# Performance work log

Hardware: AMD Instinct MI355X
Metric: run time of the kernel (lower is better)

The kernel has to match this reference:

```python
import jax, jax.numpy as jnp
import numpy as np

D_MODEL = 1024
SEQ_LEN = 4096


def setup_inputs() -> dict:
    key = jax.random.key(0)
    ks = jax.random.split(key, 7)
    s = 1.0 / np.sqrt(D_MODEL)
    return {
        "x": jax.random.normal(ks[0], (SEQ_LEN, D_MODEL), dtype=jnp.float32),
        "w_q": jax.random.normal(ks[1], (D_MODEL, D_MODEL), dtype=jnp.float32) * s,
        "b_q": jax.random.normal(ks[2], (D_MODEL,), dtype=jnp.float32) * s,
        "w_k": jax.random.normal(ks[3], (D_MODEL, D_MODEL), dtype=jnp.float32) * s,
        "b_k": jax.random.normal(ks[4], (D_MODEL,), dtype=jnp.float32) * s,
        "w_v": jax.random.normal(ks[5], (D_MODEL, D_MODEL), dtype=jnp.float32) * s,
        "b_v": jax.random.normal(ks[6], (D_MODEL,), dtype=jnp.float32) * s,
    }


def reference(x, w_q, b_q, w_k, b_k, w_v, b_v):
    # q/k/v: [S, D]; torch Linear computes x @ W.T + b, weights here stored as [D, D]
    q = x @ w_q.T + b_q
    k = x @ w_k.T + b_k
    v = x @ w_v.T + b_v
    temperature = jnp.asarray(D_MODEL, dtype=x.dtype) ** 0.5
    # scores: [S, S]
    attn = jax.nn.softmax((q / temperature) @ k.T, axis=-1)
    # dropout is identity in eval mode
    return attn @ v
```

## Files before the change

kernel.cpp:

```cpp
#include <hip/hip_runtime.h>
#include <hip/hip_bf16.h>
#include <stdint.h>

#define SEQ 4096
#define DM  1024

typedef __attribute__((ext_vector_type(8))) short  s16x8;
typedef __attribute__((ext_vector_type(8))) _Float16 h16x8;
typedef __attribute__((ext_vector_type(4))) float  f32x4;

__device__ __forceinline__ ushort f2bf(float f) {
    union { float f; uint32_t u; } x; x.f = f;
    uint32_t r = x.u + 0x7fffu + ((x.u >> 16) & 1u);
    return (ushort)(r >> 16);
}

__device__ __forceinline__ void gload16(const void* g, void* l) {
    __builtin_amdgcn_global_load_lds(
        (const __attribute__((address_space(1))) void*)g,
        (__attribute__((address_space(3))) void*)l,
        16, 0, 0);
}

__global__ __launch_bounds__(256)
void cvt_all(const float* __restrict__ x,  const float* __restrict__ wq,
             const float* __restrict__ wk, const float* __restrict__ wv,
             ushort* __restrict__ xb,  ushort* __restrict__ wqb,
             ushort* __restrict__ wkb, ushort* __restrict__ wvb)
{
    int i = blockIdx.x * 256 + threadIdx.x;
    const float* src; ushort* dst; int k;
    if (i < 1048576) { src = x; dst = xb; k = i; }
    else {
        int j = i - 1048576; int w = j >> 18; k = j & 262143;
        src = (w == 0) ? wq : (w == 1) ? wk : wv;
        dst = (w == 0) ? wqb : (w == 1) ? wkb : wvb;
    }
    float4 v = ((const float4*)src)[k];
    ushort4 o;
    o.x = f2bf(v.x); o.y = f2bf(v.y); o.z = f2bf(v.z); o.w = f2bf(v.w);
    ((ushort4*)dst)[k] = o;
}

template<int MODE>
__global__ __launch_bounds__(512, 1)
void gemm256p(const ushort* __restrict__ pA,  const ushort* __restrict__ pB,  void* __restrict__ pC,
              const ushort* __restrict__ pA2, const ushort* __restrict__ pB2, void* __restrict__ pC2,
              const ushort* __restrict__ pA3, const ushort* __restrict__ pB3, void* __restrict__ pC3,
              const float* __restrict__ pb1,  const float* __restrict__ pb2,  const float* __restrict__ pb3)
{
    constexpr int BN      = (MODE == 1) ? 128 : 256;
    constexpr int WN      = BN / 4;
    constexpr int NJ      = BN / 64;
    constexpr int LDA     = (MODE == 1) ? 4096 : 1024;
    constexpr int REG_A   = 16384;
    constexpr int REG_B   = BN * 64;
    constexpr int BUFSZ   = 2 * (REG_A + REG_B);
    constexpr int NTILES  = (MODE == 1) ? 32 : 16;
    constexpr int TOTAL_H = NTILES * 4;
    constexpr int NWG     = (MODE == 2) ? 192 : 256;

    __shared__ alignas(16) char lb[2 * BUFSZ];

    const int wg = blockIdx.x;
    const int logical = (wg & 7) * (NWG / 8) + (wg >> 3);

    int m0, n0, ldc_ = 0, biasRow = 0;
    const ushort *Ab, *Bb;
    char* Cc;
    const float* bias = nullptr;
    float scale = 1.0f;

    if constexpr (MODE == 0) {
        const int bx = logical & 15, by = logical >> 4;
        m0 = by * 256; n0 = bx * 256;
        Ab = pA + (size_t)m0 * LDA; Bb = pB + (size_t)n0 * LDA;
        Cc = (char*)pC; ldc_ = 4096;
    } else if constexpr (MODE == 1) {
        const int t = logical >> 1, ks = logical & 1;
        m0 = (t >> 3) * 256; n0 = (t & 7) * 128;
        Ab = pA + (size_t)m0 * LDA + ks * 2048;
        Bb = pB + (size_t)n0 * LDA + ks * 2048;
        Cc = (char*)pC + (size_t)ks * 8388608u;
        ldc_ = 1024;
    } else {
        const int which = logical / 64, t = logical % 64;
        if (which == 0)      { m0 = (t >> 2) * 256; n0 = (t & 3) * 256;  Ab = pA;  Bb = pB;  Cc = (char*)pC;  bias = pb1; scale = 0.03125f; ldc_ = 1024; }
        else if (which == 1) { m0 = (t >> 2) * 256; n0 = (t & 3) * 256;  Ab = pA2; Bb = pB2; Cc = (char*)pC2; bias = pb2; ldc_ = 1024; }
        else                 { m0 = (t >> 4) * 256; n0 = (t & 15) * 256; Ab = pA3; Bb = pB3; Cc = (char*)pC3; bias = pb3; biasRow = 1; ldc_ = 4096; }
        Ab += (size_t)m0 * LDA; Bb += (size_t)n0 * LDA;
    }

    const int tid = threadIdx.x;
    const int w = tid >> 6, l = tid & 63;
    const int wr = w >> 2, wc = w & 3;
    const int lm = l & 15;
    const int khb = (l >> 4) * 16;

    const int in0 = tid * 16, in1 = 8192 + tid * 16;
    const int b0 = in0 ^ (((in0 >> 9) & 1) << 5);
    const int b1 = in1 ^ (((in1 >> 9) & 1) << 5);
    const int r0_ = b0 >> 6, c0_ = (b0 & 63) >> 1;
    const int r1_ = b1 >> 6, c1_ = (b1 & 63) >> 1;

    const int swzb = ((lm >> 3) & 1) << 5;
    const int aoff = (((wr * 128 + lm) * 64 + khb) ^ swzb);
    const int boff = (((wc * WN  + lm) * 64 + khb) ^ swzb);

    f32x4 acc[8][NJ] = {};
    s16x8 bqr[NJ];

    constexpr int AR0 = 0, BR0 = REG_A, AR1 = REG_A + REG_B, BR1 = 2 * REG_A + REG_B;

#define ROFFX(reg_) ((reg_) == 0 ? AR0 : (reg_) == 1 ? BR0 : (reg_) == 2 ? AR1 : BR1)

#define STAGE_H(g) do { \
    const int hidx_ = (g) - 1, tile_ = hidx_ >> 2, reg_ = hidx_ & 3; \
    const int colb_ = tile_ * 64 + (reg_ >> 1) * 32; \
    char* dst_ = lb + (tile_ & 1) * BUFSZ + ROFFX(reg_); \
    if (reg_ & 1) { \
        gload16(Bb + (size_t)r0_ * LDA + colb_ + c0_, dst_ + in0); \
        if (BN == 256) gload16(Bb + (size_t)r1_ * LDA + colb_ + c1_, dst_ + in1); \
    } else { \
        gload16(Ab + (size_t)r0_ * LDA + colb_ + c0_, dst_ + in0); \
        gload16(Ab + (size_t)r1_ * LDA + colb_ + c1_, dst_ + in1); \
    } \
} while (0)

#define PHASE8(ph, kt2, VC) do { \
    constexpr int kk_ = (((ph) - 1) >> 1) & 1; \
    constexpr int mh_ = ((ph) - 1) & 1; \
    constexpr int rbuf_ = ((ph) <= 4) ? 0 : 1; \
    constexpr int aro_ = kk_ ? AR1 : AR0; \
    constexpr int bro_ = kk_ ? BR1 : BR0; \
    s16x8 aq[4]; \
    if (mh_ == 0) { \
        _Pragma("unroll") \
        for (int nj = 0; nj < NJ; ++nj) \
            bqr[nj] = *(const s16x8*)(lb + rbuf_ * BUFSZ + bro_ + boff + nj * 1024); \
    } \
    _Pragma("unroll") \
    for (int i = 0; i < 4; ++i) \
        aq[i] = *(const s16x8*)(lb + rbuf_ * BUFSZ + aro_ + aoff + (mh_ * 4 + i) * 1024); \
    { const int g_ = (kt2) * 8 + (ph) + 6; if (g_ <= TOTAL_H) STAGE_H(g_); } \
    asm volatile("s_waitcnt lgkmcnt(0)" ::: "memory"); \
    __builtin_amdgcn_sched_barrier(0); \
    __builtin_amdgcn_s_setprio(1); \
    _Pragma("unroll") \
    for (int i = 0; i < 4; ++i) { \
        _Pragma("unroll") \
        for (int nj = 0; nj < NJ; ++nj) \
            acc[mh_ * 4 + i][nj] = __builtin_amdgcn_mfma_f32_16x16x32_bf16( \
                aq[i], bqr[nj], acc[mh_ * 4 + i][nj], 0, 0, 0); \
    } \
    __builtin_amdgcn_s_setprio(0); \
    if ((ph) == 4 || (ph) == 8) asm volatile("s_waitcnt vmcnt(" #VC ")" ::: "memory"); \
    __builtin_amdgcn_s_barrier(); \
} while (0)

#define MPHASE(q, kt2, VC) do { \
    constexpr int kk_ = ((q) - 1) & 1; \
    constexpr int rbuf_ = ((q) <= 2) ? 0 : 1; \
    constexpr int aro_ = kk_ ? AR1 : AR0; \
    constexpr int bro_ = kk_ ? BR1 : BR0; \
    s16x8 aq[8]; \
    _Pragma("unroll") \
    for (int nj = 0; nj < NJ; ++nj) \
        bqr[nj] = *(const s16x8*)(lb + rbuf_ * BUFSZ + bro_ + boff + nj * 1024); \
    _Pragma("unroll") \
    for (int i = 0; i < 8; ++i) \
        aq[i] = *(const s16x8*)(lb + rbuf_ * BUFSZ + aro_ + aoff + i * 1024); \
    { const int g1_ = (kt2) * 8 + 2 * (q) + 5; if (g1_ <= TOTAL_H) STAGE_H(g1_); \
      const int g2_ = g1_ + 1;                 if (g2_ <= TOTAL_H) STAGE_H(g2_); } \
    asm volatile("s_waitcnt lgkmcnt(0)" ::: "memory"); \
    __builtin_amdgcn_sched_barrier(0); \
    __builtin_amdgcn_s_setprio(1); \
    _Pragma("unroll") \
    for (int i = 0; i < 8; ++i) { \
        _Pragma("unroll") \
        for (int nj = 0; nj < NJ; ++nj) \
            acc[i][nj] = __builtin_amdgcn_mfma_f32_16x16x32_bf16( \
                aq[i], bqr[nj], acc[i][nj], 0, 0, 0); \
    } \
    __builtin_amdgcn_s_setprio(0); \
    if ((q) == 2 || (q) == 4) asm volatile("s_waitcnt vmcnt(" #VC ")" ::: "memory"); \
    __builtin_amdgcn_s_barrier(); \
} while (0)

    STAGE_H(1); STAGE_H(2); STAGE_H(3); STAGE_H(4); STAGE_H(5); STAGE_H(6);
    if constexpr (MODE == 1) asm volatile("s_waitcnt vmcnt(3)" ::: "memory");
    else                     asm volatile("s_waitcnt vmcnt(4)" ::: "memory");
    __builtin_amdgcn_s_barrier();

    if constexpr (MODE == 1) {
        for (int kt2 = 0; kt2 < NTILES / 2 - 1; ++kt2) {
            MPHASE(1, kt2, 3); MPHASE(2, kt2, 3); MPHASE(3, kt2, 3); MPHASE(4, kt2, 3);
        }
        { const int kt2 = NTILES / 2 - 1;
          MPHASE(1, kt2, 0); MPHASE(2, kt2, 0); MPHASE(3, kt2, 0); MPHASE(4, kt2, 0); }
    } else {
        for (int kt2 = 0; kt2 < NTILES / 2 - 1; ++kt2) {
            PHASE8(1, kt2, 4); PHASE8(2, kt2, 4); PHASE8(3, kt2, 4); PHASE8(4, kt2, 4);
            PHASE8(5, kt2, 4); PHASE8(6, kt2, 4); PHASE8(7, kt2, 4); PHASE8(8, kt2, 4);
        }
        { const int kt2 = NTILES / 2 - 1;
          PHASE8(1, kt2, 0); PHASE8(2, kt2, 0); PHASE8(3, kt2, 0); PHASE8(4, kt2, 0);
          PHASE8(5, kt2, 0); PHASE8(6, kt2, 0); PHASE8(7, kt2, 0); PHASE8(8, kt2, 0); }
    }

    const int er0 = m0 + wr * 128 + (l >> 4) * 4;
    const int ec0 = n0 + wc * WN + lm;
#pragma unroll
    for (int mi = 0; mi < 8; ++mi) {
#pragma unroll
        for (int nj = 0; nj < NJ; ++nj) {
#pragma unroll
            for (int r = 0; r < 4; ++r) {
                const int row = er0 + mi * 16 + r;
                const int col = ec0 + nj * 16;
                if constexpr (MODE == 2) {
                    const float v = (acc[mi][nj][r] + bias[biasRow ? row : col]) * scale;
                    ((ushort*)Cc)[(size_t)row * ldc_ + col] = f2bf(v);
                } else {
                    ((_Float16*)Cc)[(size_t)row * ldc_ + col] = (_Float16)acc[mi][nj][r];
                }
            }
        }
    }
#undef MPHASE
#undef PHASE8
#undef STAGE_H
#undef ROFFX
}

__global__ __launch_bounds__(256) void softmax_rows(void* __restrict__ Sbase) {
    const int row = blockIdx.x;
    const int tid = threadIdx.x;
    const _Float16* srow = (const _Float16*)Sbase + (size_t)row * SEQ;

    float f[16];
#pragma unroll
    for (int j = 0; j < 2; ++j) {
        h16x8 v = *(const h16x8*)(srow + (size_t)(tid + j * 256) * 8);
#pragma unroll
        for (int e = 0; e < 8; ++e) f[j * 8 + e] = (float)v[e];
    }

    float m = f[0];
#pragma unroll
    for (int i = 1; i < 16; ++i) m = fmaxf(m, f[i]);
#pragma unroll
    for (int off = 32; off > 0; off >>= 1) m = fmaxf(m, __shfl_xor(m, off));

    __shared__ float redm[4], reds[4];
    const int w = tid >> 6, l = tid & 63;
    if (l == 0) redm[w] = m;
    __syncthreads();
    m = fmaxf(fmaxf(redm[0], redm[1]), fmaxf(redm[2], redm[3]));

    float s = 0.f;
#pragma unroll
    for (int i = 0; i < 16; ++i) { f[i] = __expf(f[i] - m); s += f[i]; }
#pragma unroll
    for (int off = 32; off > 0; off >>= 1) s += __shfl_xor(s, off);
    if (l == 0) reds[w] = s;
    __syncthreads();
    s = (reds[0] + reds[1]) + (reds[2] + reds[3]);
    const float inv = 1.0f / s;

    ushort* prow = (ushort*)Sbase + (size_t)row * SEQ;
#pragma unroll
    for (int j = 0; j < 2; ++j) {
        s16x8 o;
#pragma unroll
        for (int e = 0; e < 8; ++e) o[e] = (short)f2bf(f[j * 8 + e] * inv);
        *(s16x8*)(prow + (size_t)(tid + j * 256) * 8) = o;
    }
}

__global__ __launch_bounds__(256)
void reduce2(const _Float16* __restrict__ p0, const _Float16* __restrict__ p1,
             float* __restrict__ out)
{
    const size_t i = (size_t)(blockIdx.x * 256 + threadIdx.x) * 8;
    h16x8 a = *(const h16x8*)(p0 + i);
    h16x8 b = *(const h16x8*)(p1 + i);
    float4 o0, o1;
    o0.x = (float)a[0] + (float)b[0]; o0.y = (float)a[1] + (float)b[1];
    o0.z = (float)a[2] + (float)b[2]; o0.w = (float)a[3] + (float)b[3];
    o1.x = (float)a[4] + (float)b[4]; o1.y = (float)a[5] + (float)b[5];
    o1.z = (float)a[6] + (float)b[6]; o1.w = (float)a[7] + (float)b[7];
    *(float4*)(out + i) = o0;
    *(float4*)(out + i + 4) = o1;
}

extern "C" void kernel_launch(void* const* d_in, const int* in_sizes, int n_in,
                              void* d_out, int out_size, void* d_ws, size_t ws_size,
                              hipStream_t stream)
{
    const float* x  = (const float*)d_in[0];
    const float* wq = (const float*)d_in[1];
    const float* bq = (const float*)d_in[2];
    const float* wk = (const float*)d_in[3];
    const float* bk = (const float*)d_in[4];
    const float* wv = (const float*)d_in[5];
    const float* bv = (const float*)d_in[6];

    char* ws = (char*)d_ws;
    const size_t MB = 1024 * 1024;
    ushort*   Qb  = (ushort*)(ws);
    ushort*   Kb  = (ushort*)(ws + 8 * MB);
    ushort*   Vt  = (ushort*)(ws + 16 * MB);
    void*     Sm  = (void*)(ws + 24 * MB);
    ushort*   P   = (ushort*)(ws + 24 * MB);
    ushort*   xb  = (ushort*)(ws + 24 * MB);
    ushort*   wqb = (ushort*)(ws + 32 * MB);
    ushort*   wkb = (ushort*)(ws + 34 * MB);
    ushort*   wvb = (ushort*)(ws + 36 * MB);
    _Float16* Pp  = (_Float16*)(ws);

    cvt_all<<<dim3(7168), dim3(256), 0, stream>>>(x, wq, wk, wv, xb, wqb, wkb, wvb);

    gemm256p<2><<<dim3(192), dim3(512), 0, stream>>>(
        xb, wqb, Qb, xb, wkb, Kb, wvb, xb, Vt, bq, bk, bv);

    gemm256p<0><<<dim3(256), dim3(512), 0, stream>>>(
        Qb, Kb, Sm, nullptr, nullptr, nullptr, nullptr, nullptr, nullptr,
        nullptr, nullptr, nullptr);

    softmax_rows<<<dim3(SEQ), dim3(256), 0, stream>>>(Sm);

    gemm256p<1><<<dim3(256), dim3(512), 0, stream>>>(
        P, Vt, Pp, nullptr, nullptr, nullptr, nullptr, nullptr, nullptr,
        nullptr, nullptr, nullptr);

    reduce2<<<dim3(2048), dim3(256), 0, stream>>>(Pp, Pp + (size_t)4096 * 1024,
                                                  (float*)d_out);
}
```

Before: 133.1 us.

## Use 128x128-tile GEMM kernel for QK^T and PV, grid-stride softmax

Adds a new gemm128p kernel (256 threads, 128x128 tiles, two blocks per CU) and uses it for the QK^T score GEMM and the split-K PV GEMM, replacing the 256-tile MODE 0/1 paths. The original 256-tile kernel is now kept only for the fused QKV projection. Softmax now runs on 2048 blocks that each loop over two rows. Smaller tiles give more workgroups and better occupancy on the many CUs, at the cost of less operand reuse per tile and more global and LDS traffic.

```diff
diff --git a/kernel.cpp b/kernel.cpp
--- a/kernel.cpp
+++ b/kernel.cpp
@@ -49,16 +49,16 @@
               const ushort* __restrict__ pA3, const ushort* __restrict__ pB3, void* __restrict__ pC3,
               const float* __restrict__ pb1,  const float* __restrict__ pb2,  const float* __restrict__ pb3)
 {
-    constexpr int BN      = (MODE == 1) ? 128 : 256;
+    constexpr int BN      = 256;
     constexpr int WN      = BN / 4;
     constexpr int NJ      = BN / 64;
-    constexpr int LDA     = (MODE == 1) ? 4096 : 1024;
+    constexpr int LDA     = 1024;
     constexpr int REG_A   = 16384;
     constexpr int REG_B   = BN * 64;
     constexpr int BUFSZ   = 2 * (REG_A + REG_B);
-    constexpr int NTILES  = (MODE == 1) ? 32 : 16;
+    constexpr int NTILES  = 16;
     constexpr int TOTAL_H = NTILES * 4;
-    constexpr int NWG     = (MODE == 2) ? 192 : 256;
+    constexpr int NWG     = 192;
 
     __shared__ alignas(16) char lb[2 * BUFSZ];
 
@@ -71,19 +71,7 @@
     const float* bias = nullptr;
     float scale = 1.0f;
 
-    if constexpr (MODE == 0) {
-        const int bx = logical & 15, by = logical >> 4;
-        m0 = by * 256; n0 = bx * 256;
-        Ab = pA + (size_t)m0 * LDA; Bb = pB + (size_t)n0 * LDA;
-        Cc = (char*)pC; ldc_ = 4096;
-    } else if constexpr (MODE == 1) {
-        const int t = logical >> 1, ks = logical & 1;
-        m0 = (t >> 3) * 256; n0 = (t & 7) * 128;
-        Ab = pA + (size_t)m0 * LDA + ks * 2048;
-        Bb = pB + (size_t)n0 * LDA + ks * 2048;
-        Cc = (char*)pC + (size_t)ks * 8388608u;
-        ldc_ = 1024;
-    } else {
+    {
         const int which = logical / 64, t = logical % 64;
         if (which == 0)      { m0 = (t >> 2) * 256; n0 = (t & 3) * 256;  Ab = pA;  Bb = pB;  Cc = (char*)pC;  bias = pb1; scale = 0.03125f; ldc_ = 1024; }
         else if (which == 1) { m0 = (t >> 2) * 256; n0 = (t & 3) * 256;  Ab = pA2; Bb = pB2; Cc = (char*)pC2; bias = pb2; ldc_ = 1024; }
@@ -120,7 +108,7 @@
     char* dst_ = lb + (tile_ & 1) * BUFSZ + ROFFX(reg_); \
     if (reg_ & 1) { \
         gload16(Bb + (size_t)r0_ * LDA + colb_ + c0_, dst_ + in0); \
-        if (BN == 256) gload16(Bb + (size_t)r1_ * LDA + colb_ + c1_, dst_ + in1); \
+        gload16(Bb + (size_t)r1_ * LDA + colb_ + c1_, dst_ + in1); \
     } else { \
         gload16(Ab + (size_t)r0_ * LDA + colb_ + c0_, dst_ + in0); \
         gload16(Ab + (size_t)r1_ * LDA + colb_ + c1_, dst_ + in1); \
@@ -158,27 +146,123 @@
     __builtin_amdgcn_s_barrier(); \
 } while (0)
 
-#define MPHASE(q, kt2, VC) do { \
+    STAGE_H(1); STAGE_H(2); STAGE_H(3); STAGE_H(4); STAGE_H(5); STAGE_H(6);
+    asm volatile("s_waitcnt vmcnt(4)" ::: "memory");
+    __builtin_amdgcn_s_barrier();
+
+    for (int kt2 = 0; kt2 < NTILES / 2 - 1; ++kt2) {
+        PHASE8(1, kt2, 4); PHASE8(2, kt2, 4); PHASE8(3, kt2, 4); PHASE8(4, kt2, 4);
+        PHASE8(5, kt2, 4); PHASE8(6, kt2, 4); PHASE8(7, kt2, 4); PHASE8(8, kt2, 4);
+    }
+    { const int kt2 = NTILES / 2 - 1;
+      PHASE8(1, kt2, 0); PHASE8(2, kt2, 0); PHASE8(3, kt2, 0); PHASE8(4, kt2, 0);
+      PHASE8(5, kt2, 0); PHASE8(6, kt2, 0); PHASE8(7, kt2, 0); PHASE8(8, kt2, 0); }
+
+    const int er0 = m0 + wr * 128 + (l >> 4) * 4;
+    const int ec0 = n0 + wc * WN + lm;
+#pragma unroll
+    for (int mi = 0; mi < 8; ++mi) {
+#pragma unroll
+        for (int nj = 0; nj < NJ; ++nj) {
+#pragma unroll
+            for (int r = 0; r < 4; ++r) {
+                const int row = er0 + mi * 16 + r;
+                const int col = ec0 + nj * 16;
+                const float v = (acc[mi][nj][r] + bias[biasRow ? row : col]) * scale;
+                ((ushort*)Cc)[(size_t)row * ldc_ + col] = f2bf(v);
+            }
+        }
+    }
+#undef PHASE8
+#undef STAGE_H
+#undef ROFFX
+}
+
+template<int IS_PV>
+__global__ __launch_bounds__(256, 2)
+void gemm128p(const ushort* __restrict__ A, const ushort* __restrict__ B,
+              _Float16* __restrict__ C)
+{
+    constexpr int LDA     = IS_PV ? 4096 : 1024;
+    constexpr int LDC     = IS_PV ? 1024 : 4096;
+    constexpr int NTILES  = IS_PV ? 32 : 16;
+    constexpr int TOTAL_H = NTILES * 4;
+    constexpr int REG     = 8192;
+    constexpr int BUFSZ   = 4 * REG;
+    __shared__ alignas(16) char lb[2 * BUFSZ];
+
+    const int wg = blockIdx.x;
+    int m0, n0;
+    const ushort *Ab, *Bb;
+    _Float16* Cc;
+    if constexpr (!IS_PV) {
+        const int logical = (wg & 7) * 128 + (wg >> 3);
+        const int bx = logical & 31, by = logical >> 5;
+        m0 = by * 128; n0 = bx * 128;
+        Ab = A + (size_t)m0 * LDA; Bb = B + (size_t)n0 * LDA; Cc = C;
+    } else {
+        const int logical = (wg & 7) * 64 + (wg >> 3);
+        const int ks = logical & 1, t = logical >> 1;
+        const int by = t >> 3, bx = t & 7;
+        m0 = by * 128; n0 = bx * 128;
+        Ab = A + (size_t)m0 * LDA + ks * 2048;
+        Bb = B + (size_t)n0 * LDA + ks * 2048;
+        Cc = C + (size_t)ks * 4194304u;
+    }
+
+    const int tid = threadIdx.x;
+    const int w = tid >> 6, l = tid & 63;
+    const int wm = (w >> 1) * 64, wn = (w & 1) * 64;
+    const int lm = l & 15;
+    const int khb = (l >> 4) * 16;
+
+    const int in0 = tid * 16, in1 = 4096 + tid * 16;
+    const int b0 = in0 ^ (((in0 >> 9) & 1) << 5);
+    const int b1 = in1 ^ (((in1 >> 9) & 1) << 5);
+    const int r0_ = b0 >> 6, c0_ = (b0 & 63) >> 1;
+    const int r1_ = b1 >> 6, c1_ = (b1 & 63) >> 1;
+
+    const int swzb = ((lm >> 3) & 1) << 5;
+    const int aoff = ((wm + lm) * 64 + khb) ^ swzb;
+    const int boff = ((wn + lm) * 64 + khb) ^ swzb;
+
+    f32x4 acc[4][4] = {};
+    s16x8 bqr[4];
+
+    constexpr int AR0 = 0, BR0 = REG, AR1 = 2 * REG, BR1 = 3 * REG;
+
+#define ROFF3(reg_) ((reg_) == 0 ? AR0 : (reg_) == 1 ? BR0 : (reg_) == 2 ? AR1 : BR1)
+
+#define STAGE3(g) do { \
+    const int hidx_ = (g) - 1, tile_ = hidx_ >> 2, reg_ = hidx_ & 3; \
+    const int colb_ = tile_ * 64 + (reg_ >> 1) * 32; \
+    char* dst_ = lb + (tile_ & 1) * BUFSZ + ROFF3(reg_); \
+    const ushort* mp_ = (reg_ & 1) ? Bb : Ab; \
+    gload16(mp_ + (size_t)r0_ * LDA + colb_ + c0_, dst_ + in0); \
+    gload16(mp_ + (size_t)r1_ * LDA + colb_ + c1_, dst_ + in1); \
+} while (0)
+
+#define MP3(q, kt2, VC) do { \
     constexpr int kk_ = ((q) - 1) & 1; \
     constexpr int rbuf_ = ((q) <= 2) ? 0 : 1; \
     constexpr int aro_ = kk_ ? AR1 : AR0; \
     constexpr int bro_ = kk_ ? BR1 : BR0; \
-    s16x8 aq[8]; \
+    s16x8 aq[4]; \
     _Pragma("unroll") \
-    for (int nj = 0; nj < NJ; ++nj) \
+    for (int nj = 0; nj < 4; ++nj) \
         bqr[nj] = *(const s16x8*)(lb + rbuf_ * BUFSZ + bro_ + boff + nj * 1024); \
     _Pragma("unroll") \
-    for (int i = 0; i < 8; ++i) \
+    for (int i = 0; i < 4; ++i) \
         aq[i] = *(const s16x8*)(lb + rbuf_ * BUFSZ + aro_ + aoff + i * 1024); \
-    { const int g1_ = (kt2) * 8 + 2 * (q) + 5; if (g1_ <= TOTAL_H) STAGE_H(g1_); \
-      const int g2_ = g1_ + 1;                 if (g2_ <= TOTAL_H) STAGE_H(g2_); } \
+    { const int g1_ = (kt2) * 8 + 2 * (q) + 5; if (g1_ <= TOTAL_H) STAGE3(g1_); \
+      const int g2_ = g1_ + 1;                 if (g2_ <= TOTAL_H) STAGE3(g2_); } \
     asm volatile("s_waitcnt lgkmcnt(0)" ::: "memory"); \
     __builtin_amdgcn_sched_barrier(0); \
     __builtin_amdgcn_s_setprio(1); \
     _Pragma("unroll") \
-    for (int i = 0; i < 8; ++i) { \
+    for (int i = 0; i < 4; ++i) { \
         _Pragma("unroll") \
-        for (int nj = 0; nj < NJ; ++nj) \
+        for (int nj = 0; nj < 4; ++nj) \
             acc[i][nj] = __builtin_amdgcn_mfma_f32_16x16x32_bf16( \
                 aq[i], bqr[nj], acc[i][nj], 0, 0, 0); \
     } \
@@ -187,94 +271,76 @@
     __builtin_amdgcn_s_barrier(); \
 } while (0)
 
-    STAGE_H(1); STAGE_H(2); STAGE_H(3); STAGE_H(4); STAGE_H(5); STAGE_H(6);
-    if constexpr (MODE == 1) asm volatile("s_waitcnt vmcnt(3)" ::: "memory");
-    else                     asm volatile("s_waitcnt vmcnt(4)" ::: "memory");
+    STAGE3(1); STAGE3(2); STAGE3(3); STAGE3(4); STAGE3(5); STAGE3(6);
+    asm volatile("s_waitcnt vmcnt(4)" ::: "memory");
     __builtin_amdgcn_s_barrier();
 
-    if constexpr (MODE == 1) {
-        for (int kt2 = 0; kt2 < NTILES / 2 - 1; ++kt2) {
-            MPHASE(1, kt2, 3); MPHASE(2, kt2, 3); MPHASE(3, kt2, 3); MPHASE(4, kt2, 3);
+    for (int kt2 = 0; kt2 < NTILES / 2 - 1; ++kt2) {
+        MP3(1, kt2, 4); MP3(2, kt2, 4); MP3(3, kt2, 4); MP3(4, kt2, 4);
+    }
+    { const int kt2 = NTILES / 2 - 1;
+      MP3(1, kt2, 0); MP3(2, kt2, 0); MP3(3, kt2, 0); MP3(4, kt2, 0); }
+
+    const int er0 = m0 + wm + ((l >> 4) << 2);
+    const int ec0 = n0 + wn + lm;
+#pragma unroll
+    for (int mi = 0; mi < 4; ++mi)
+#pragma unroll
+        for (int nj = 0; nj < 4; ++nj)
+#pragma unroll
+            for (int r = 0; r < 4; ++r)
+                Cc[(size_t)(er0 + mi * 16 + r) * LDC + ec0 + nj * 16] =
+                    (_Float16)acc[mi][nj][r];
+#undef MP3
+#undef STAGE3
+#undef ROFF3
+}
+
+__global__ __launch_bounds__(256) void softmax_rows(void* __restrict__ Sbase) {
+    const int tid = threadIdx.x;
+    const int w = tid >> 6, l = tid & 63;
+    __shared__ float redm[4], reds[4];
+
+    for (int row = blockIdx.x; row < SEQ; row += 2048) {
+        const _Float16* srow = (const _Float16*)Sbase + (size_t)row * SEQ;
+
+        float f[16];
+#pragma unroll
+        for (int j = 0; j < 2; ++j) {
+            h16x8 v = *(const h16x8*)(srow + (size_t)(tid + j * 256) * 8);
+#pragma unroll
+            for (int e = 0; e < 8; ++e) f[j * 8 + e] = (float)v[e];
         }
-        { const int kt2 = NTILES / 2 - 1;
-          MPHASE(1, kt2, 0); MPHASE(2, kt2, 0); MPHASE(3, kt2, 0); MPHASE(4, kt2, 0); }
-    } else {
-        for (int kt2 = 0; kt2 < NTILES / 2 - 1; ++kt2) {
-            PHASE8(1, kt2, 4); PHASE8(2, kt2, 4); PHASE8(3, kt2, 4); PHASE8(4, kt2, 4);
-            PHASE8(5, kt2, 4); PHASE8(6, kt2, 4); PHASE8(7, kt2, 4); PHASE8(8, kt2, 4);
+
+        float m = f[0];
+#pragma unroll
+        for (int i = 1; i < 16; ++i) m = fmaxf(m, f[i]);
+#pragma unroll
+        for (int off = 32; off > 0; off >>= 1) m = fmaxf(m, __shfl_xor(m, off));
+
+        if (l == 0) redm[w] = m;
+        __syncthreads();
+        m = fmaxf(fmaxf(redm[0], redm[1]), fmaxf(redm[2], redm[3]));
+
+        float s = 0.f;
+#pragma unroll
+        for (int i = 0; i < 16; ++i) { f[i] = __expf(f[i] - m); s += f[i]; }
+#pragma unroll
+        for (int off = 32; off > 0; off >>= 1) s += __shfl_xor(s, off);
+        if (l == 0) reds[w] = s;
+        __syncthreads();
+        s = (reds[0] + reds[1]) + (reds[2] + reds[3]);
+        const float inv = 1.0f / s;
+
+        ushort* prow = (ushort*)Sbase + (size_t)row * SEQ;
+#pragma unroll
+        for (int j = 0; j < 2; ++j) {
+            s16x8 o;
+#pragma unroll
+            for (int e = 0; e < 8; ++e) o[e] = (short)f2bf(f[j * 8 + e] * inv);
+            *(s16x8*)(prow + (size_t)(tid + j * 256) * 8) = o;
         }
-        { const int kt2 = NTILES / 2 - 1;
-          PHASE8(1, kt2, 0); PHASE8(2, kt2, 0); PHASE8(3, kt2, 0); PHASE8(4, kt2, 0);
-          PHASE8(5, kt2, 0); PHASE8(6, kt2, 0); PHASE8(7, kt2, 0); PHASE8(8, kt2, 0); }
-    }
-
-    const int er0 = m0 + wr * 128 + (l >> 4) * 4;
-    const int ec0 = n0 + wc * WN + lm;
-#pragma unroll
-    for (int mi = 0; mi < 8; ++mi) {
-#pragma unroll
-        for (int nj = 0; nj < NJ; ++nj) {
-#pragma unroll
-            for (int r = 0; r < 4; ++r) {
-                const int row = er0 + mi * 16 + r;
-                const int col = ec0 + nj * 16;
-                if constexpr (MODE == 2) {
-                    const float v = (acc[mi][nj][r] + bias[biasRow ? row : col]) * scale;
-                    ((ushort*)Cc)[(size_t)row * ldc_ + col] = f2bf(v);
-                } else {
-                    ((_Float16*)Cc)[(size_t)row * ldc_ + col] = (_Float16)acc[mi][nj][r];
-                }
-            }
-        }
-    }
-#undef MPHASE
-#undef PHASE8
-#undef STAGE_H
-#undef ROFFX
-}
-
-__global__ __launch_bounds__(256) void softmax_rows(void* __restrict__ Sbase) {
-    const int row = blockIdx.x;
-    const int tid = threadIdx.x;
-    const _Float16* srow = (const _Float16*)Sbase + (size_t)row * SEQ;
-
-    float f[16];
-#pragma unroll
-    for (int j = 0; j < 2; ++j) {
-        h16x8 v = *(const h16x8*)(srow + (size_t)(tid + j * 256) * 8);
-#pragma unroll
-        for (int e = 0; e < 8; ++e) f[j * 8 + e] = (float)v[e];
-    }
-
-    float m = f[0];
-#pragma unroll
-    for (int i = 1; i < 16; ++i) m = fmaxf(m, f[i]);
-#pragma unroll
-    for (int off = 32; off > 0; off >>= 1) m = fmaxf(m, __shfl_xor(m, off));
-
-    __shared__ float redm[4], reds[4];
-    const int w = tid >> 6, l = tid & 63;
-    if (l == 0) redm[w] = m;
-    __syncthreads();
-    m = fmaxf(fmaxf(redm[0], redm[1]), fmaxf(redm[2], redm[3]));
-
-    float s = 0.f;
-#pragma unroll
-    for (int i = 0; i < 16; ++i) { f[i] = __expf(f[i] - m); s += f[i]; }
-#pragma unroll
-    for (int off = 32; off > 0; off >>= 1) s += __shfl_xor(s, off);
-    if (l == 0) reds[w] = s;
-    __syncthreads();
-    s = (reds[0] + reds[1]) + (reds[2] + reds[3]);
-    const float inv = 1.0f / s;
-
-    ushort* prow = (ushort*)Sbase + (size_t)row * SEQ;
-#pragma unroll
-    for (int j = 0; j < 2; ++j) {
-        s16x8 o;
-#pragma unroll
-        for (int e = 0; e < 8; ++e) o[e] = (short)f2bf(f[j * 8 + e] * inv);
-        *(s16x8*)(prow + (size_t)(tid + j * 256) * 8) = o;
+        __syncthreads();
     }
 }
 
@@ -324,15 +390,11 @@
     gemm256p<2><<<dim3(192), dim3(512), 0, stream>>>(
         xb, wqb, Qb, xb, wkb, Kb, wvb, xb, Vt, bq, bk, bv);
 
-    gemm256p<0><<<dim3(256), dim3(512), 0, stream>>>(
-        Qb, Kb, Sm, nullptr, nullptr, nullptr, nullptr, nullptr, nullptr,
-        nullptr, nullptr, nullptr);
-
-    softmax_rows<<<dim3(SEQ), dim3(256), 0, stream>>>(Sm);
-
-    gemm256p<1><<<dim3(256), dim3(512), 0, stream>>>(
-        P, Vt, Pp, nullptr, nullptr, nullptr, nullptr, nullptr, nullptr,
-        nullptr, nullptr, nullptr);
+    gemm128p<0><<<dim3(1024), dim3(256), 0, stream>>>(Qb, Kb, (_Float16*)Sm);
+
+    softmax_rows<<<dim3(2048), dim3(256), 0, stream>>>(Sm);
+
+    gemm128p<1><<<dim3(512), dim3(256), 0, stream>>>(P, Vt, Pp);
 
     reduce2<<<dim3(2048), dim3(256), 0, stream>>>(Pp, Pp + (size_t)4096 * 1024,
                                                   (float*)d_out);
```

New measurement: 146.7 us. 10.2% more time.
